# Kernel tuning notes

Hardware: AMD Instinct MI355X
Metric: run time of the kernel (lower is better)

The kernel has to match this reference:

```python
import jax, jax.numpy as jnp
import numpy as np

SEQ, BATCH, IN, H = 2048, 1024, 10, 20


def setup_inputs() -> dict:
    key = jax.random.key(0)
    ks = jax.random.split(key, 11)
    s = 1.0 / np.sqrt(H)  # PyTorch LSTM init range
    u = lambda k, shape: jax.random.uniform(k, shape, jnp.float32, -s, s)
    return {
        "x": jax.random.normal(ks[0], (SEQ, BATCH, IN), jnp.float32),
        "h0": jax.random.normal(ks[1], (2, BATCH, H), jnp.float32),
        "c0": jax.random.normal(ks[2], (2, BATCH, H), jnp.float32),
        "w_ih_f": u(ks[3], (4 * H, IN)),
        "w_hh_f": u(ks[4], (4 * H, H)),
        "b_ih_f": u(ks[5], (4 * H,)),
        "b_hh_f": u(ks[6], (4 * H,)),
        "w_ih_b": u(ks[7], (4 * H, IN)),
        "w_hh_b": u(ks[8], (4 * H, H)),
        "b_ih_b": u(ks[9], (4 * H,)),
        "b_hh_b": u(ks[10], (4 * H,)),
    }


def _scan_dir(x_proj, h0, c0, w_hh):
    # x_proj: [seq, batch, 4H] precomputed input projection + biases
    def step(carry, g_in):
        h, c = carry
        g = g_in + h @ w_hh.T  # [batch, 4H]
        i, f, gg, o = jnp.split(g, 4, axis=-1)  # PyTorch gate order i,f,g,o
        c = jax.nn.sigmoid(f) * c + jax.nn.sigmoid(i) * jnp.tanh(gg)
        h = jax.nn.sigmoid(o) * jnp.tanh(c)
        return (h, c), h

    (hT, cT), hs = jax.lax.scan(step, (h0, c0), x_proj)
    return hs, hT, cT


def reference(x, h0, c0, w_ih_f, w_hh_f, b_ih_f, b_hh_f, w_ih_b, w_hh_b, b_ih_b, b_hh_b):
    # forward direction
    xf = jnp.einsum('sbi,gi->sbg', x, w_ih_f) + (b_ih_f + b_hh_f)
    hs_f, hT_f, cT_f = _scan_dir(xf, h0[0], c0[0], w_hh_f)
    # backward direction: scan over time-reversed sequence, then flip outputs
    xb = jnp.einsum('sbi,gi->sbg', x[::-1], w_ih_b) + (b_ih_b + b_hh_b)
    hs_b, hT_b, cT_b = _scan_dir(xb, h0[1], c0[1], w_hh_b)
    hs_b = hs_b[::-1]
    out = jnp.concatenate([hs_f, hs_b], axis=-1)  # [seq, batch, 2H]
    h_n = jnp.stack([hT_f, hT_b])  # [2, batch, H]
    c_n = jnp.stack([cT_f, cT_b])
    return out, h_n, c_n
```

## Files before the change

kernel.cpp:

```cpp
#include <hip/hip_runtime.h>

namespace {

constexpr int SEQ = 2048, BATCH = 1024, IN = 10, H = 20;
constexpr int XS  = 32;
constexpr int XRW = 8;
constexpr float L2E = 1.4426950408889634f;
constexpr float K2  = -2.0f * L2E;

typedef _Float16 h2t __attribute__((ext_vector_type(2)));

__device__ __forceinline__ float rcpf(float x) { return __builtin_amdgcn_rcpf(x); }
__device__ __forceinline__ float xp2(float x)  { return __builtin_amdgcn_exp2f(x); }

__device__ __forceinline__ int pk(float a, float b) {
    auto v = __builtin_amdgcn_cvt_pkrtz(a, b);
    int i; __builtin_memcpy(&i, &v, 4); return i;
}
__device__ __forceinline__ float dot2(int a, int b, float c) {
    h2t ha, hb; __builtin_memcpy(&ha, &a, 4); __builtin_memcpy(&hb, &b, 4);
    return __builtin_amdgcn_fdot2(ha, hb, c, false);
}
__device__ __forceinline__ float dpp_x1(float v) {
    int i; __builtin_memcpy(&i, &v, 4);
    int r = __builtin_amdgcn_update_dpp(0, i, 0xB1, 0xF, 0xF, true);
    float f; __builtin_memcpy(&f, &r, 4); return f;
}
__device__ __forceinline__ float dpp_x2(float v) {
    int i; __builtin_memcpy(&i, &v, 4);
    int r = __builtin_amdgcn_update_dpp(0, i, 0x4E, 0xF, 0xF, true);
    float f; __builtin_memcpy(&f, &r, 4); return f;
}

__launch_bounds__(64)
__global__ void lstm_bidir(const float* __restrict__ x,
                           const float* __restrict__ h0,
                           const float* __restrict__ c0,
                           const float* __restrict__ w_ih_f, const float* __restrict__ w_hh_f,
                           const float* __restrict__ b_ih_f, const float* __restrict__ b_hh_f,
                           const float* __restrict__ w_ih_b, const float* __restrict__ w_hh_b,
                           const float* __restrict__ b_ih_b, const float* __restrict__ b_hh_b,
                           float* __restrict__ out, float* __restrict__ h_n, float* __restrict__ c_n)
{
    const int dir  = blockIdx.y;
    const int b    = blockIdx.x;
    const int lane = threadIdx.x;
    const int u    = lane >> 1;
    const int gp   = lane & 1;
    const int ur   = (u < H) ? u : (H - 1);
    const bool red = (gp == 0) && (u < H);

    const float* w_ih = dir ? w_ih_b : w_ih_f;
    const float* w_hh = dir ? w_hh_b : w_hh_f;
    const float* bi   = dir ? b_ih_b : b_ih_f;
    const float* bh   = dir ? b_hh_b : b_hh_f;

    __shared__ __align__(16) int xlds[2][XS * XRW];
    __shared__ __align__(16) int hl[96];

    const int g0 = gp * 2 * H + ur, g1 = g0 + H;
    const float sc0 = gp ? K2 : (-L2E);
    const float sc1 = -L2E;
    const float na0 = gp ? (2.0f * K2) : 1.0f;
    const float nd0 = gp ? (-K2) : 0.0f;

    int wh[2][10], wi[2][5]; float bias[2];
    #pragma unroll
    for (int k = 0; k < 10; ++k) {
        wh[0][k] = pk(w_hh[g0 * H + 2 * k] * sc0, w_hh[g0 * H + 2 * k + 1] * sc0);
        wh[1][k] = pk(w_hh[g1 * H + 2 * k] * sc1, w_hh[g1 * H + 2 * k + 1] * sc1);
    }
    #pragma unroll
    for (int k = 0; k < 5; ++k) {
        wi[0][k] = pk(w_ih[g0 * IN + 2 * k] * sc0, w_ih[g0 * IN + 2 * k + 1] * sc0);
        wi[1][k] = pk(w_ih[g1 * IN + 2 * k] * sc1, w_ih[g1 * IN + 2 * k + 1] * sc1);
    }
    bias[0] = (bi[g0] + bh[g0]) * sc0;
    bias[1] = (bi[g1] + bh[g1]) * sc1;

    float c  = c0[(dir * BATCH + b) * H + ur] * K2;
    float hv = h0[(dir * BATCH + b) * H + ur];

    const bool wok  = ((lane & 2) == 0) && (u < H);
    const int  hoff = wok ? (lane >> 2) : (16 + lane);
    hl[hoff] = pk(hv, dpp_x2(hv));

    const float*    xbase = x + b * IN;
    const ptrdiff_t xstep = dir ? -(ptrdiff_t)(BATCH * IN) : (ptrdiff_t)(BATCH * IN);
    const size_t    xoff0 = (size_t)(dir ? SEQ - 1 : 0) * (BATCH * IN);

    float2 pend[3];
    auto issue_chunk = [&](int s0) {
        #pragma unroll
        for (int i = 0; i < 3; ++i) {
            const int e = lane + 64 * i;
            if (i < 2 || lane < 32) {
                const int ss = e / 5, j = e % 5;
                pend[i] = *(const float2*)(xbase + xoff0 + (ptrdiff_t)(s0 + ss) * xstep + 2 * j);
            }
        }
    };
    auto write_chunk = [&](int buf) {
        #pragma unroll
        for (int i = 0; i < 3; ++i) {
            const int e = lane + 64 * i;
            if (i < 2 || lane < 32)
                xlds[buf][(e / 5) * XRW + (e % 5)] = pk(pend[i].x, pend[i].y);
        }
    };

    issue_chunk(0);  write_chunk(0);
    issue_chunk(XS);

    float*          optr  = out + (size_t)(dir ? SEQ - 1 : 0) * (BATCH * 2 * H) + b * (2 * H) + dir * H + ur;
    const ptrdiff_t ostep = dir ? -(ptrdiff_t)(BATCH * 2 * H) : (ptrdiff_t)(BATCH * 2 * H);

    for (int s0 = 0; s0 < SEQ; s0 += XS) {
        const int buf = (s0 >> 5) & 1;
        #pragma unroll 4
        for (int ss = 0; ss < XS; ++ss) {
            const int* xr = &xlds[buf][ss * XRW];
            const int4 xA = *(const int4*)xr;
            const int  x4 = xr[4];
            const int  xq[5] = { xA.x, xA.y, xA.z, xA.w, x4 };

            const int4 hA = *(const int4*)&hl[0];
            const int4 hB = *(const int4*)&hl[4];
            const int2 hC = *(const int2*)&hl[8];
            const int  hp[10] = { hA.x, hA.y, hA.z, hA.w, hB.x, hB.y, hB.z, hB.w, hC.x, hC.y };

            float a0 = bias[0], a1 = bias[1], p0 = 0.0f, p1 = 0.0f;
            #pragma unroll
            for (int k = 0; k < 3; ++k) {
                a0 = dot2(xq[k], wi[0][k], a0);
                a1 = dot2(xq[k], wi[1][k], a1);
            }
            #pragma unroll
            for (int k = 3; k < 5; ++k) {
                p0 = dot2(xq[k], wi[0][k], p0);
                p1 = dot2(xq[k], wi[1][k], p1);
            }
            #pragma unroll
            for (int k = 0; k < 5; ++k) {
                a0 = dot2(hp[k],     wh[0][k],     a0);
                a1 = dot2(hp[k],     wh[1][k],     a1);
                p0 = dot2(hp[k + 5], wh[0][k + 5], p0);
                p1 = dot2(hp[k + 5], wh[1][k + 5], p1);
            }
            a0 += p0;  a1 += p1;

            const float n0 = fmaf(na0, rcpf(1.0f + xp2(a0)), nd0);
            const float n1 = rcpf(1.0f + xp2(a1));

            const float m0 = dpp_x1(n0);
            const float m1 = dpp_x1(n1);
            const float F  = gp ? m1 : n1;
            c = fmaf(F, c, n0 * m0);
            const float th = fmaf(2.0f, rcpf(1.0f + xp2(c)), -1.0f);
            const float o  = gp ? n1 : m1;
            hv = o * th;

            hl[hoff] = pk(hv, dpp_x2(hv));
            if (red) __builtin_nontemporal_store(hv, optr);
            optr += ostep;
        }
        if (s0 + XS < SEQ) {
            write_chunk(buf ^ 1);
            if (s0 + 2 * XS < SEQ) issue_chunk(s0 + 2 * XS);
        }
    }

    if (red) {
        h_n[(dir * BATCH + b) * H + ur] = hv;
        c_n[(dir * BATCH + b) * H + ur] = c * (1.0f / K2);
    }
}

}

extern "C" void kernel_launch(void* const* d_in, const int* in_sizes, int n_in,
                              void* d_out, int out_size, void* d_ws, size_t ws_size,
                              hipStream_t stream)
{
    const float* x      = (const float*)d_in[0];
    const float* h0     = (const float*)d_in[1];
    const float* c0     = (const float*)d_in[2];
    const float* w_ih_f = (const float*)d_in[3];
    const float* w_hh_f = (const float*)d_in[4];
    const float* b_ih_f = (const float*)d_in[5];
    const float* b_hh_f = (const float*)d_in[6];
    const float* w_ih_b = (const float*)d_in[7];
    const float* w_hh_b = (const float*)d_in[8];
    const float* b_ih_b = (const float*)d_in[9];
    const float* b_hh_b = (const float*)d_in[10];

    float* out = (float*)d_out;
    float* h_n = out + (size_t)SEQ * BATCH * 2 * H;
    float* c_n = h_n + (size_t)2 * BATCH * H;

    dim3 grid(BATCH, 2), block(64);
    hipLaunchKernelGGL(lstm_bidir, grid, block, 0, stream,
                       x, h0, c0, w_ih_f, w_hh_f, b_ih_f, b_hh_f,
                       w_ih_b, w_hh_b, b_ih_b, b_hh_b, out, h_n, c_n);
}
```

Baseline: 567.9 us.

## Interleave two batch chains per wavefront to hide recurrent latency

Each 64-lane block now processes two batch elements with independent recurrences, interleaving their per-step dot products, activations and LDS h exchanges so one chain's latency overlaps the other's work. The grid is halved and the x staging layout widened so both rows' inputs share one chunk. This trades fewer blocks (less occupancy-based latency hiding) and more registers for instruction-level parallelism inside each wave.

```diff
diff --git a/kernel.cpp b/kernel.cpp
--- a/kernel.cpp
+++ b/kernel.cpp
@@ -4,7 +4,7 @@
 
 constexpr int SEQ = 2048, BATCH = 1024, IN = 10, H = 20;
 constexpr int XS  = 32;
-constexpr int XRW = 8;
+constexpr int XRW = 16;
 constexpr float L2E = 1.4426950408889634f;
 constexpr float K2  = -2.0f * L2E;
 
@@ -43,20 +43,25 @@
                            float* __restrict__ out, float* __restrict__ h_n, float* __restrict__ c_n)
 {
     const int dir  = blockIdx.y;
-    const int b    = blockIdx.x;
+    const int bA   = blockIdx.x * 2;
+    const int bB   = bA + 1;
     const int lane = threadIdx.x;
     const int u    = lane >> 1;
     const int gp   = lane & 1;
     const int ur   = (u < H) ? u : (H - 1);
     const bool red = (gp == 0) && (u < H);
 
+    const bool okp  = ((lane & 2) == 0) && (u < H);
+    const int  offA = okp ? (lane >> 2) : (32 + lane);
+    const int  offB = okp ? (16 + (lane >> 2)) : (96 + lane);
+
     const float* w_ih = dir ? w_ih_b : w_ih_f;
     const float* w_hh = dir ? w_hh_b : w_hh_f;
     const float* bi   = dir ? b_ih_b : b_ih_f;
     const float* bh   = dir ? b_hh_b : b_hh_f;
 
     __shared__ __align__(16) int xlds[2][XS * XRW];
-    __shared__ __align__(16) int hl[96];
+    __shared__ __align__(16) int hl[160];
 
     const int g0 = gp * 2 * H + ur, g1 = g0 + H;
     const float sc0 = gp ? K2 : (-L2E);
@@ -78,91 +83,101 @@
     bias[0] = (bi[g0] + bh[g0]) * sc0;
     bias[1] = (bi[g1] + bh[g1]) * sc1;
 
-    float c  = c0[(dir * BATCH + b) * H + ur] * K2;
-    float hv = h0[(dir * BATCH + b) * H + ur];
-
-    const bool wok  = ((lane & 2) == 0) && (u < H);
-    const int  hoff = wok ? (lane >> 2) : (16 + lane);
-    hl[hoff] = pk(hv, dpp_x2(hv));
-
-    const float*    xbase = x + b * IN;
+    float cA = c0[(dir * BATCH + bA) * H + ur] * K2;
+    float hA = h0[(dir * BATCH + bA) * H + ur];
+    float cB = c0[(dir * BATCH + bB) * H + ur] * K2;
+    float hB = h0[(dir * BATCH + bB) * H + ur];
+
+    hl[offA] = pk(hA, dpp_x2(hA));
+    hl[offB] = pk(hB, dpp_x2(hB));
+
+    const float*    xbase = x + bA * IN;
     const ptrdiff_t xstep = dir ? -(ptrdiff_t)(BATCH * IN) : (ptrdiff_t)(BATCH * IN);
     const size_t    xoff0 = (size_t)(dir ? SEQ - 1 : 0) * (BATCH * IN);
 
-    float2 pend[3];
+    float2 pend[5];
     auto issue_chunk = [&](int s0) {
         #pragma unroll
-        for (int i = 0; i < 3; ++i) {
-            const int e = lane + 64 * i;
-            if (i < 2 || lane < 32) {
-                const int ss = e / 5, j = e % 5;
-                pend[i] = *(const float2*)(xbase + xoff0 + (ptrdiff_t)(s0 + ss) * xstep + 2 * j);
-            }
+        for (int i = 0; i < 5; ++i) {
+            const int e  = lane + 64 * i;
+            const int ss = e / 10, j = e % 10;
+            pend[i] = *(const float2*)(xbase + xoff0 + (ptrdiff_t)(s0 + ss) * xstep + 2 * j);
         }
     };
     auto write_chunk = [&](int buf) {
         #pragma unroll
-        for (int i = 0; i < 3; ++i) {
-            const int e = lane + 64 * i;
-            if (i < 2 || lane < 32)
-                xlds[buf][(e / 5) * XRW + (e % 5)] = pk(pend[i].x, pend[i].y);
+        for (int i = 0; i < 5; ++i) {
+            const int e  = lane + 64 * i;
+            const int ss = e / 10, j = e % 10;
+            xlds[buf][ss * XRW + j + (j >= 5 ? 3 : 0)] = pk(pend[i].x, pend[i].y);
         }
     };
 
     issue_chunk(0);  write_chunk(0);
     issue_chunk(XS);
 
-    float*          optr  = out + (size_t)(dir ? SEQ - 1 : 0) * (BATCH * 2 * H) + b * (2 * H) + dir * H + ur;
     const ptrdiff_t ostep = dir ? -(ptrdiff_t)(BATCH * 2 * H) : (ptrdiff_t)(BATCH * 2 * H);
+    float* optrA = out + (size_t)(dir ? SEQ - 1 : 0) * (BATCH * 2 * H) + bA * (2 * H) + dir * H + ur;
+    float* optrB = optrA + 2 * H;
+
+    auto chain_step = [&](const int* xr, int hb, float& c, float& hv) -> int {
+        const int4 xA4 = *(const int4*)xr;
+        const int  x4  = xr[4];
+        const int  xq[5] = { xA4.x, xA4.y, xA4.z, xA4.w, x4 };
+
+        const int4 h04 = *(const int4*)&hl[hb];
+        const int4 h48 = *(const int4*)&hl[hb + 4];
+        const int2 h89 = *(const int2*)&hl[hb + 8];
+        const int  hp[10] = { h04.x, h04.y, h04.z, h04.w, h48.x, h48.y, h48.z, h48.w, h89.x, h89.y };
+
+        float a0 = bias[0], a1 = bias[1], p0 = 0.0f, p1 = 0.0f;
+        #pragma unroll
+        for (int k = 0; k < 3; ++k) {
+            a0 = dot2(xq[k], wi[0][k], a0);
+            a1 = dot2(xq[k], wi[1][k], a1);
+        }
+        #pragma unroll
+        for (int k = 3; k < 5; ++k) {
+            p0 = dot2(xq[k], wi[0][k], p0);
+            p1 = dot2(xq[k], wi[1][k], p1);
+        }
+        #pragma unroll
+        for (int k = 0; k < 5; ++k) {
+            a0 = dot2(hp[k],     wh[0][k],     a0);
+            a1 = dot2(hp[k],     wh[1][k],     a1);
+            p0 = dot2(hp[k + 5], wh[0][k + 5], p0);
+            p1 = dot2(hp[k + 5], wh[1][k + 5], p1);
+        }
+        a0 += p0;  a1 += p1;
+
+        const float n0 = fmaf(na0, rcpf(1.0f + xp2(a0)), nd0);
+        const float n1 = rcpf(1.0f + xp2(a1));
+        const float m0 = dpp_x1(n0);
+        const float m1 = dpp_x1(n1);
+        const float F  = gp ? m1 : n1;
+        c = fmaf(F, c, n0 * m0);
+        const float th = fmaf(2.0f, rcpf(1.0f + xp2(c)), -1.0f);
+        const float o  = gp ? n1 : m1;
+        hv = o * th;
+        return pk(hv, dpp_x2(hv));
+    };
 
     for (int s0 = 0; s0 < SEQ; s0 += XS) {
         const int buf = (s0 >> 5) & 1;
-        #pragma unroll 4
+        #pragma unroll 2
         for (int ss = 0; ss < XS; ++ss) {
             const int* xr = &xlds[buf][ss * XRW];
-            const int4 xA = *(const int4*)xr;
-            const int  x4 = xr[4];
-            const int  xq[5] = { xA.x, xA.y, xA.z, xA.w, x4 };
-
-            const int4 hA = *(const int4*)&hl[0];
-            const int4 hB = *(const int4*)&hl[4];
-            const int2 hC = *(const int2*)&hl[8];
-            const int  hp[10] = { hA.x, hA.y, hA.z, hA.w, hB.x, hB.y, hB.z, hB.w, hC.x, hC.y };
-
-            float a0 = bias[0], a1 = bias[1], p0 = 0.0f, p1 = 0.0f;
-            #pragma unroll
-            for (int k = 0; k < 3; ++k) {
-                a0 = dot2(xq[k], wi[0][k], a0);
-                a1 = dot2(xq[k], wi[1][k], a1);
+            const int pairA = chain_step(xr,     0,  cA, hA);
+            const int pairB = chain_step(xr + 8, 16, cB, hB);
+
+            hl[offA] = pairA;
+            hl[offB] = pairB;
+
+            if (red) {
+                __builtin_nontemporal_store(hA, optrA);
+                __builtin_nontemporal_store(hB, optrB);
             }
-            #pragma unroll
-            for (int k = 3; k < 5; ++k) {
-                p0 = dot2(xq[k], wi[0][k], p0);
-                p1 = dot2(xq[k], wi[1][k], p1);
-            }
-            #pragma unroll
-            for (int k = 0; k < 5; ++k) {
-                a0 = dot2(hp[k],     wh[0][k],     a0);
-                a1 = dot2(hp[k],     wh[1][k],     a1);
-                p0 = dot2(hp[k + 5], wh[0][k + 5], p0);
-                p1 = dot2(hp[k + 5], wh[1][k + 5], p1);
-            }
-            a0 += p0;  a1 += p1;
-
-            const float n0 = fmaf(na0, rcpf(1.0f + xp2(a0)), nd0);
-            const float n1 = rcpf(1.0f + xp2(a1));
-
-            const float m0 = dpp_x1(n0);
-            const float m1 = dpp_x1(n1);
-            const float F  = gp ? m1 : n1;
-            c = fmaf(F, c, n0 * m0);
-            const float th = fmaf(2.0f, rcpf(1.0f + xp2(c)), -1.0f);
-            const float o  = gp ? n1 : m1;
-            hv = o * th;
-
-            hl[hoff] = pk(hv, dpp_x2(hv));
-            if (red) __builtin_nontemporal_store(hv, optr);
-            optr += ostep;
+            optrA += ostep;  optrB += ostep;
         }
         if (s0 + XS < SEQ) {
             write_chunk(buf ^ 1);
@@ -171,8 +186,10 @@
     }
 
     if (red) {
-        h_n[(dir * BATCH + b) * H + ur] = hv;
-        c_n[(dir * BATCH + b) * H + ur] = c * (1.0f / K2);
+        h_n[(dir * BATCH + bA) * H + ur] = hA;
+        c_n[(dir * BATCH + bA) * H + ur] = cA * (1.0f / K2);
+        h_n[(dir * BATCH + bB) * H + ur] = hB;
+        c_n[(dir * BATCH + bB) * H + ur] = cB * (1.0f / K2);
     }
 }
 
@@ -198,7 +215,7 @@
     float* h_n = out + (size_t)SEQ * BATCH * 2 * H;
     float* c_n = h_n + (size_t)2 * BATCH * H;
 
-    dim3 grid(BATCH, 2), block(64);
+    dim3 grid(BATCH / 2, 2), block(64);
     hipLaunchKernelGGL(lstm_bidir, grid, block, 0, stream,
                        x, h0, c0, w_ih_f, w_hh_f, b_ih_f, b_hh_f,
                        w_ih_b, w_hh_b, b_ih_b, b_hh_b, out, h_n, c_n);
```

After: 679.7 us. 1.2x slower.
